# Optimization experiments

Hardware: AMD Instinct MI355X
Metric: run time of the kernel (lower is better)

## Reference

```python
import jax, jax.numpy as jnp
import numpy as np

EPS = 1e-5

def layer_norm(x, g, b):
    m = x.mean(-1, keepdims=True)
    v = ((x - m) ** 2).mean(-1, keepdims=True)
    return (x - m) * jax.lax.rsqrt(v + EPS) * g + b

def setup_inputs() -> dict:
    key = jax.random.key(0)
    ks = jax.random.split(key, 12)
    H = 2048; E = 2048; I = 2048; N = 32
    A = (H + E) // 2  # attention hidden = 2048
    s = lambda fan: 1.0 / np.sqrt(fan)
    inp = {
        "input":   jax.random.normal(ks[0], (I,), jnp.float32),
        "hiddens": jax.random.normal(ks[1], (N, H), jnp.float32),
        "cells":   jax.random.normal(ks[2], (N, H), jnp.float32),
        "external":jax.random.normal(ks[3], (E,), jnp.float32),
        # weights (torch nn.Linear layout: [out, in]); LN enabled -> no biases on linears
        "W_ai":   jax.random.uniform(ks[4], (A, H + E), jnp.float32, -s(H+E), s(H+E)),
        "W_attn": jax.random.uniform(ks[5], (1, A), jnp.float32, -s(A), s(A)),
        "W_merge":jax.random.uniform(ks[6], (H, H), jnp.float32, -s(H), s(H)),
        "W_iou":  jax.random.uniform(ks[7], (3 * H, I + H), jnp.float32, -s(I+H), s(I+H)),
        "W_fi":   jax.random.uniform(ks[8], (H, I), jnp.float32, -s(I), s(I)),
        "W_fh":   jax.random.uniform(ks[9], (H, H), jnp.float32, -s(H), s(H)),
        "g_merge": jnp.ones((H,), jnp.float32), "b_merge": jnp.zeros((H,), jnp.float32),
        "g_f": jnp.ones((H,), jnp.float32), "b_f": jnp.zeros((H,), jnp.float32),
        "g_i": jnp.ones((H,), jnp.float32), "b_i": jnp.zeros((H,), jnp.float32),
        "g_o": jnp.ones((H,), jnp.float32), "b_o": jnp.zeros((H,), jnp.float32),
        "g_u": jnp.ones((H,), jnp.float32), "b_u": jnp.zeros((H,), jnp.float32),
        "g_c": jnp.ones((H,), jnp.float32), "b_c": jnp.zeros((H,), jnp.float32),
    }
    return inp

def reference(input, hiddens, cells, external,
              W_ai, W_attn, W_merge, W_iou, W_fi, W_fh,
              g_merge, b_merge, g_f, b_f, g_i, b_i, g_o, b_o, g_u, b_u, g_c, b_c):
    N, H = hiddens.shape
    # forget-gate preactivations: [H] + [N,H] -> [N,H]
    f_lin = input @ W_fi.T + hiddens @ W_fh.T
    # attentive merge over children
    ext = jnp.broadcast_to(external, (N, external.shape[0]))
    ai = jnp.tanh(jnp.concatenate([hiddens, ext], axis=1) @ W_ai.T)       # [N, (H+E)//2]
    attn = jax.nn.softmax(ai @ W_attn.T, axis=0)                          # [N, 1]
    merged = (hiddens * attn).sum(0)                                      # [H]
    merge_hidden = jnp.tanh(layer_norm(merged @ W_merge.T, g_merge, b_merge))
    # i/o/u gates from [input ; merged_hidden]
    iou = jnp.concatenate([input, merge_hidden]) @ W_iou.T                # [3H]
    i_l, o_l, u_l = jnp.split(iou, 3)
    f = jax.nn.sigmoid(layer_norm(f_lin, g_f, b_f))                       # [N,H]
    i = jax.nn.sigmoid(layer_norm(i_l, g_i, b_i))
    o = jax.nn.sigmoid(layer_norm(o_l, g_o, b_o))
    u = jnp.tanh(layer_norm(u_l, g_u, b_u))                               # dropout=0 -> identity
    new_cell = layer_norm(i * u + (f * cells).sum(0), g_c, b_c)           # [H]
    new_h = o * jnp.tanh(new_cell)
    return new_h, new_cell
```

## Files before the change

### kernel.cpp

```cpp
#include <hip/hip_runtime.h>
#include <hip/hip_bf16.h>

typedef __bf16 bf16_t;
typedef __attribute__((ext_vector_type(8))) __bf16 bf16x8;
typedef __attribute__((ext_vector_type(4))) float f32x4;

#define EPSF 1e-5f

__global__ __launch_bounds__(256) void s1_mega(
    const float* __restrict__ hiddens, const float* __restrict__ external,
    const float* __restrict__ input,
    const float* __restrict__ W_ai, const float* __restrict__ W_fh,
    const float* __restrict__ W_fi, const float* __restrict__ W_attn,
    float* __restrict__ lp, float* __restrict__ fh_out, float* __restrict__ fi_out)
{
    __shared__ float red[4][16][16];
    __shared__ float ejs[4][16];

    int b    = blockIdx.x;
    int tid  = threadIdx.x;
    int wave = tid >> 6;
    int lane = tid & 63;

    if (b < 512) {
        bool is_ai = (b < 256);
        int  bb    = is_ai ? b : b - 256;
        int  jt    = bb & 127;
        int  nt    = bb >> 7;
        int  l15   = lane & 15;
        int  quad  = lane >> 4;
        int  k0    = wave * 512;
        int  wstride = is_ai ? 4096 : 2048;
        const float* W = is_ai ? W_ai : W_fh;

        const float* ap = hiddens + (size_t)(nt * 16 + l15) * 2048 + quad * 8 + k0;
        const float* bp = W + (size_t)(jt * 16 + l15) * wstride + quad * 8 + k0;

        f32x4 acc = {0.f, 0.f, 0.f, 0.f};
        float ejacc = 0.f;

        if (is_ai) {
            const float* ep = bp + 2048;
            const float* xp = external + quad * 8 + k0;
            for (int k = 0; k < 512; k += 32) {
                float4 a0 = *(const float4*)(ap + k);
                float4 a1 = *(const float4*)(ap + k + 4);
                float4 b0 = *(const float4*)(bp + k);
                float4 b1 = *(const float4*)(bp + k + 4);
                bf16x8 av, bv;
                av[0]=(bf16_t)a0.x; av[1]=(bf16_t)a0.y; av[2]=(bf16_t)a0.z; av[3]=(bf16_t)a0.w;
                av[4]=(bf16_t)a1.x; av[5]=(bf16_t)a1.y; av[6]=(bf16_t)a1.z; av[7]=(bf16_t)a1.w;
                bv[0]=(bf16_t)b0.x; bv[1]=(bf16_t)b0.y; bv[2]=(bf16_t)b0.z; bv[3]=(bf16_t)b0.w;
                bv[4]=(bf16_t)b1.x; bv[5]=(bf16_t)b1.y; bv[6]=(bf16_t)b1.z; bv[7]=(bf16_t)b1.w;
                acc = __builtin_amdgcn_mfma_f32_16x16x32_bf16(av, bv, acc, 0, 0, 0);
                float4 e0 = *(const float4*)(ep + k);
                float4 e1 = *(const float4*)(ep + k + 4);
                float4 x0 = *(const float4*)(xp + k);
                float4 x1 = *(const float4*)(xp + k + 4);
                ejacc += e0.x*x0.x + e0.y*x0.y + e0.z*x0.z + e0.w*x0.w
                       + e1.x*x1.x + e1.y*x1.y + e1.z*x1.z + e1.w*x1.w;
            }
            ejacc += __shfl_xor(ejacc, 16, 64);
            ejacc += __shfl_xor(ejacc, 32, 64);
            if (quad == 0) ejs[wave][l15] = ejacc;
        } else {
            for (int k = 0; k < 512; k += 32) {
                float4 a0 = *(const float4*)(ap + k);
                float4 a1 = *(const float4*)(ap + k + 4);
                float4 b0 = *(const float4*)(bp + k);
                float4 b1 = *(const float4*)(bp + k + 4);
                bf16x8 av, bv;
                av[0]=(bf16_t)a0.x; av[1]=(bf16_t)a0.y; av[2]=(bf16_t)a0.z; av[3]=(bf16_t)a0.w;
                av[4]=(bf16_t)a1.x; av[5]=(bf16_t)a1.y; av[6]=(bf16_t)a1.z; av[7]=(bf16_t)a1.w;
                bv[0]=(bf16_t)b0.x; bv[1]=(bf16_t)b0.y; bv[2]=(bf16_t)b0.z; bv[3]=(bf16_t)b0.w;
                bv[4]=(bf16_t)b1.x; bv[5]=(bf16_t)b1.y; bv[6]=(bf16_t)b1.z; bv[7]=(bf16_t)b1.w;
                acc = __builtin_amdgcn_mfma_f32_16x16x32_bf16(av, bv, acc, 0, 0, 0);
            }
        }

        #pragma unroll
        for (int r = 0; r < 4; ++r) red[wave][quad * 4 + r][l15] = acc[r];
        __syncthreads();

        int row = tid >> 4, col = tid & 15;
        float s = red[0][row][col] + red[1][row][col] + red[2][row][col] + red[3][row][col];

        if (is_ai) {
            float ej = ejs[0][col] + ejs[1][col] + ejs[2][col] + ejs[3][col];
            float lg = tanhf(s + ej) * W_attn[jt * 16 + col];
            lg += __shfl_xor(lg, 1, 64);
            lg += __shfl_xor(lg, 2, 64);
            lg += __shfl_xor(lg, 4, 64);
            lg += __shfl_xor(lg, 8, 64);
            if (col == 0) lp[jt * 32 + nt * 16 + row] = lg;
        } else {
            fh_out[(size_t)(nt * 16 + row) * 2048 + jt * 16 + col] = s;
        }
    } else {
        int b2 = b - 512;
        #pragma unroll
        for (int r = 0; r < 4; ++r) {
            int row = b2 * 16 + wave * 4 + r;
            const float4* wp = (const float4*)(W_fi + (size_t)row * 2048) + lane;
            const float4* xp = (const float4*)input + lane;
            float acc2 = 0.f;
            #pragma unroll
            for (int k = 0; k < 512; k += 64) {
                float4 w = wp[k];
                float4 v = xp[k];
                acc2 += w.x*v.x + w.y*v.y + w.z*v.z + w.w*v.w;
            }
            #pragma unroll
            for (int off = 32; off; off >>= 1) acc2 += __shfl_down(acc2, off, 64);
            if (lane == 0) fi_out[row] = acc2;
        }
    }
}

__global__ __launch_bounds__(256) void s2_mega(
    const float* __restrict__ fi, const float* __restrict__ fh,
    const float* __restrict__ lp, const float* __restrict__ hiddens,
    float* __restrict__ frs, float* __restrict__ merged)
{
    __shared__ float s1[256], s2[256];
    int b = blockIdx.x, t = threadIdx.x;

    if (b < 32) {
        int n = b;
        float sum = 0.f, sq = 0.f;
        #pragma unroll
        for (int i = 0; i < 8; ++i) {
            int h = t * 8 + i;
            float v = fi[h] + fh[n * 2048 + h];
            sum += v; sq += v * v;
        }
        s1[t] = sum; s2[t] = sq;
        __syncthreads();
        for (int off = 128; off; off >>= 1) {
            if (t < off) { s1[t] += s1[t + off]; s2[t] += s2[t + off]; }
            __syncthreads();
        }
        if (t == 0) {
            const float inv = 1.f / 2048.f;
            float mean = s1[0] * inv;
            frs[n * 2]     = mean;
            frs[n * 2 + 1] = rsqrtf(s2[0] * inv - mean * mean + EPSF);
        }
    } else {
        __shared__ float lred[32][8];
        __shared__ float attnw[32];
        int n = t >> 3, sl = t & 7;
        float p = 0.f;
        #pragma unroll
        for (int m = 0; m < 16; ++m) p += lp[(sl * 16 + m) * 32 + n];
        lred[n][sl] = p;
        __syncthreads();
        if (sl == 0) {
            float lg = 0.f;
            #pragma unroll
            for (int m = 0; m < 8; ++m) lg += lred[n][m];
            lred[n][0] = lg;
        }
        __syncthreads();
        if (t < 32) {
            float mx = -1e30f;
            for (int m = 0; m < 32; ++m) mx = fmaxf(mx, lred[m][0]);
            float ssum = 0.f;
            for (int m = 0; m < 32; ++m) ssum += expf(lred[m][0] - mx);
            attnw[t] = expf(lred[t][0] - mx) / ssum;
        }
        __syncthreads();
        int h = (b - 32) * 256 + t;
        float acc = 0.f;
        #pragma unroll 8
        for (int n2 = 0; n2 < 32; ++n2) acc += attnw[n2] * hiddens[n2 * 2048 + h];
        merged[h] = acc;
    }
}

__global__ __launch_bounds__(256) void s3_mega(
    const float* __restrict__ W_merge, const float* __restrict__ merged,
    const float* __restrict__ fi, const float* __restrict__ fh,
    const float* __restrict__ frs, const float* __restrict__ gf,
    const float* __restrict__ bf_, const float* __restrict__ cells,
    float* __restrict__ mm, float* __restrict__ fc)
{
    int b = blockIdx.x, t = threadIdx.x;
    if (b < 512) {
        int row  = b * 4 + (t >> 6);
        int lane = t & 63;
        const float4* wp = (const float4*)(W_merge + (size_t)row * 2048) + lane;
        const float4* xp = (const float4*)merged + lane;
        float acc = 0.f;
        #pragma unroll
        for (int k = 0; k < 512; k += 64) {
            float4 w = wp[k];
            float4 v = xp[k];
            acc += w.x*v.x + w.y*v.y + w.z*v.z + w.w*v.w;
        }
        #pragma unroll
        for (int off = 32; off; off >>= 1) acc += __shfl_down(acc, off, 64);
        if (lane == 0) mm[row] = acc;
    } else {
        int h = (b - 512) * 256 + t;
        float g = gf[h], bb = bf_[h], f_i = fi[h];
        float acc = 0.f;
        for (int n = 0; n < 32; ++n) {
            float v = (f_i + fh[n * 2048 + h] - frs[n * 2]) * frs[n * 2 + 1] * g + bb;
            float f = 1.f / (1.f + expf(-v));
            acc += f * cells[n * 2048 + h];
        }
        fc[h] = acc;
    }
}

__global__ __launch_bounds__(256) void s4_iou(
    const float* __restrict__ W_iou, const float* __restrict__ mm,
    const float* __restrict__ input, const float* __restrict__ g,
    const float* __restrict__ bvec, float* __restrict__ iou)
{
    __shared__ float xcat[4096];
    __shared__ float s1[256], s2[256];
    int b = blockIdx.x, t = threadIdx.x;

    float v[8]; float sum = 0.f, sq = 0.f;
    #pragma unroll
    for (int i = 0; i < 8; ++i) {
        v[i] = mm[t * 8 + i]; sum += v[i]; sq += v[i] * v[i];
    }
    s1[t] = sum; s2[t] = sq;
    __syncthreads();
    for (int off = 128; off; off >>= 1) {
        if (t < off) { s1[t] += s1[t + off]; s2[t] += s2[t + off]; }
        __syncthreads();
    }
    const float inv = 1.f / 2048.f;
    float mean = s1[0] * inv;
    float r = rsqrtf(s2[0] * inv - mean * mean + EPSF);
    #pragma unroll
    for (int i = 0; i < 8; ++i) {
        int h = t * 8 + i;
        xcat[h]        = input[h];
        xcat[2048 + h] = tanhf((v[i] - mean) * r * g[h] + bvec[h]);
    }
    __syncthreads();

    int wave = t >> 6, lane = t & 63;
    #pragma unroll
    for (int rr = 0; rr < 4; ++rr) {
        int row = b * 16 + wave * 4 + rr;
        const float4* wp = (const float4*)(W_iou + (size_t)row * 4096) + lane;
        const float4* xp = (const float4*)xcat + lane;
        float acc = 0.f;
        #pragma unroll
        for (int k = 0; k < 1024; k += 64) {
            float4 w = wp[k];
            float4 x = xp[k];
            acc += w.x*x.x + w.y*x.y + w.z*x.z + w.w*x.w;
        }
        #pragma unroll
        for (int off = 32; off; off >>= 1) acc += __shfl_down(acc, off, 64);
        if (lane == 0) iou[row] = acc;
    }
}

__global__ __launch_bounds__(256) void s5_tail(
    const float* __restrict__ iou, const float* __restrict__ fc,
    const float* __restrict__ gi, const float* __restrict__ bi,
    const float* __restrict__ go, const float* __restrict__ bo,
    const float* __restrict__ gu, const float* __restrict__ bu,
    const float* __restrict__ gc, const float* __restrict__ bc,
    float* __restrict__ out)
{
    __shared__ float sA[6][256];
    int t = threadIdx.x;
    float vi[8], vo[8], vu[8];
    float si = 0, qi = 0, so = 0, qo = 0, su = 0, qu = 0;
    #pragma unroll
    for (int i = 0; i < 8; ++i) {
        int h = t * 8 + i;
        vi[i] = iou[h]; vo[i] = iou[2048 + h]; vu[i] = iou[4096 + h];
        si += vi[i]; qi += vi[i] * vi[i];
        so += vo[i]; qo += vo[i] * vo[i];
        su += vu[i]; qu += vu[i] * vu[i];
    }
    sA[0][t] = si; sA[1][t] = qi; sA[2][t] = so;
    sA[3][t] = qo; sA[4][t] = su; sA[5][t] = qu;
    __syncthreads();
    for (int off = 128; off; off >>= 1) {
        if (t < off) {
            #pragma unroll
            for (int c = 0; c < 6; ++c) sA[c][t] += sA[c][t + off];
        }
        __syncthreads();
    }
    const float inv = 1.f / 2048.f;
    float mi = sA[0][0] * inv, ri = rsqrtf(sA[1][0] * inv - mi * mi + EPSF);
    float mo = sA[2][0] * inv, ro = rsqrtf(sA[3][0] * inv - mo * mo + EPSF);
    float mu = sA[4][0] * inv, ru = rsqrtf(sA[5][0] * inv - mu * mu + EPSF);
    __syncthreads();

    float o_[8], v_[8];
    float sv = 0, qv = 0;
    #pragma unroll
    for (int i = 0; i < 8; ++i) {
        int h = t * 8 + i;
        float ivl = 1.f / (1.f + expf(-((vi[i] - mi) * ri * gi[h] + bi[h])));
        o_[i]     = 1.f / (1.f + expf(-((vo[i] - mo) * ro * go[h] + bo[h])));
        float uvl = tanhf((vu[i] - mu) * ru * gu[h] + bu[h]);
        v_[i] = ivl * uvl + fc[h];
        sv += v_[i]; qv += v_[i] * v_[i];
    }
    sA[0][t] = sv; sA[1][t] = qv;
    __syncthreads();
    for (int off = 128; off; off >>= 1) {
        if (t < off) { sA[0][t] += sA[0][t + off]; sA[1][t] += sA[1][t + off]; }
        __syncthreads();
    }
    float mc = sA[0][0] * inv, rc = rsqrtf(sA[1][0] * inv - mc * mc + EPSF);
    #pragma unroll
    for (int i = 0; i < 8; ++i) {
        int h = t * 8 + i;
        float nc = (v_[i] - mc) * rc * gc[h] + bc[h];
        float nh = o_[i] * tanhf(nc);
        out[h]        = nh;
        out[2048 + h] = nc;
    }
}

extern "C" void kernel_launch(void* const* d_in, const int* in_sizes, int n_in,
                              void* d_out, int out_size, void* d_ws, size_t ws_size,
                              hipStream_t stream)
{
    const float* input    = (const float*)d_in[0];
    const float* hiddens  = (const float*)d_in[1];
    const float* cells    = (const float*)d_in[2];
    const float* external = (const float*)d_in[3];
    const float* W_ai     = (const float*)d_in[4];
    const float* W_attn   = (const float*)d_in[5];
    const float* W_merge  = (const float*)d_in[6];
    const float* W_iou    = (const float*)d_in[7];
    const float* W_fi     = (const float*)d_in[8];
    const float* W_fh     = (const float*)d_in[9];
    const float* g_merge  = (const float*)d_in[10];
    const float* b_merge  = (const float*)d_in[11];
    const float* g_f      = (const float*)d_in[12];
    const float* b_f      = (const float*)d_in[13];
    const float* g_i      = (const float*)d_in[14];
    const float* b_i      = (const float*)d_in[15];
    const float* g_o      = (const float*)d_in[16];
    const float* b_o      = (const float*)d_in[17];
    const float* g_u      = (const float*)d_in[18];
    const float* b_u      = (const float*)d_in[19];
    const float* g_c      = (const float*)d_in[20];
    const float* b_c      = (const float*)d_in[21];

    float* ws = (float*)d_ws;
    float* ws_fh     = ws;
    float* ws_fi     = ws + 65536;
    float* ws_lp     = ws + 67584;
    float* ws_frs    = ws + 71680;
    float* ws_merged = ws + 71744;
    float* ws_mm     = ws + 73792;
    float* ws_fc     = ws + 75840;
    float* ws_iou    = ws + 77888;
    float* out = (float*)d_out;

    s1_mega<<<640, 256, 0, stream>>>(hiddens, external, input,
                                     W_ai, W_fh, W_fi, W_attn,
                                     ws_lp, ws_fh, ws_fi);
    s2_mega<<<40, 256, 0, stream>>>(ws_fi, ws_fh, ws_lp, hiddens,
                                    ws_frs, ws_merged);
    s3_mega<<<520, 256, 0, stream>>>(W_merge, ws_merged, ws_fi, ws_fh,
                                     ws_frs, g_f, b_f, cells, ws_mm, ws_fc);
    s4_iou<<<384, 256, 0, stream>>>(W_iou, ws_mm, input, g_merge, b_merge, ws_iou);
    s5_tail<<<1, 256, 0, stream>>>(ws_iou, ws_fc, g_i, b_i, g_o, b_o,
                                   g_u, b_u, g_c, b_c, out);
}
```

Before: 279.7 us.

## Fuse five stage kernels into one cooperative kernel with grid syncs

Replaces the five separate stage launches with a single cooperative kernel of 512 blocks that separates the stages with grid.sync(). The goal is to remove per-launch overhead and the gaps between kernels in this latency-bound, memory-streaming workload. Each MFMA block now computes both 16-row halves of the batch, reusing each loaded weight tile twice, and the per-block row counts of the GEMV stages are rebalanced to fit the smaller grid. In exchange the grid is capped at the co-resident limit of 2 blocks per CU, some stages leave many blocks idle, and each grid barrier has its own cost.

Result: slower. 534.8 us (+91.2%).

```diff
diff --git a/kernel.cpp b/kernel.cpp
--- a/kernel.cpp
+++ b/kernel.cpp
@@ -1,5 +1,8 @@
 #include <hip/hip_runtime.h>
 #include <hip/hip_bf16.h>
+#include <hip/hip_cooperative_groups.h>
+
+namespace cg = cooperative_groups;
 
 typedef __bf16 bf16_t;
 typedef __attribute__((ext_vector_type(8))) __bf16 bf16x8;
@@ -7,52 +10,64 @@
 
 #define EPSF 1e-5f
 
-__global__ __launch_bounds__(256) void s1_mega(
-    const float* __restrict__ hiddens, const float* __restrict__ external,
-    const float* __restrict__ input,
-    const float* __restrict__ W_ai, const float* __restrict__ W_fh,
-    const float* __restrict__ W_fi, const float* __restrict__ W_attn,
-    float* __restrict__ lp, float* __restrict__ fh_out, float* __restrict__ fi_out)
+#define CVT8(dst, s0, s1)                                                      \
+    dst[0]=(bf16_t)s0.x; dst[1]=(bf16_t)s0.y; dst[2]=(bf16_t)s0.z; dst[3]=(bf16_t)s0.w; \
+    dst[4]=(bf16_t)s1.x; dst[5]=(bf16_t)s1.y; dst[6]=(bf16_t)s1.z; dst[7]=(bf16_t)s1.w;
+
+__global__ __launch_bounds__(256, 2) void mega(
+    const float* __restrict__ input, const float* __restrict__ hiddens,
+    const float* __restrict__ cells, const float* __restrict__ external,
+    const float* __restrict__ W_ai, const float* __restrict__ W_attn,
+    const float* __restrict__ W_merge, const float* __restrict__ W_iou,
+    const float* __restrict__ W_fi, const float* __restrict__ W_fh,
+    const float* __restrict__ g_merge, const float* __restrict__ b_merge,
+    const float* __restrict__ g_f, const float* __restrict__ b_f,
+    const float* __restrict__ g_i, const float* __restrict__ b_i,
+    const float* __restrict__ g_o, const float* __restrict__ b_o,
+    const float* __restrict__ g_u, const float* __restrict__ b_u,
+    const float* __restrict__ g_c, const float* __restrict__ b_c,
+    float* __restrict__ lp, float* __restrict__ fh_out, float* __restrict__ fi_out,
+    float* __restrict__ frs, float* __restrict__ merged, float* __restrict__ mm,
+    float* __restrict__ fc, float* __restrict__ iou, float* __restrict__ out)
 {
-    __shared__ float red[4][16][16];
-    __shared__ float ejs[4][16];
-
-    int b    = blockIdx.x;
-    int tid  = threadIdx.x;
-    int wave = tid >> 6;
-    int lane = tid & 63;
-
-    if (b < 512) {
-        bool is_ai = (b < 256);
-        int  bb    = is_ai ? b : b - 256;
-        int  jt    = bb & 127;
-        int  nt    = bb >> 7;
-        int  l15   = lane & 15;
-        int  quad  = lane >> 4;
-        int  k0    = wave * 512;
-        int  wstride = is_ai ? 4096 : 2048;
-        const float* W = is_ai ? W_ai : W_fh;
-
-        const float* ap = hiddens + (size_t)(nt * 16 + l15) * 2048 + quad * 8 + k0;
-        const float* bp = W + (size_t)(jt * 16 + l15) * wstride + quad * 8 + k0;
-
-        f32x4 acc = {0.f, 0.f, 0.f, 0.f};
-        float ejacc = 0.f;
+    cg::grid_group grid = cg::this_grid();
+    __shared__ __align__(16) float sm[4608];
+
+    const int b    = blockIdx.x;
+    const int tid  = threadIdx.x;
+    const int wave = tid >> 6;
+    const int lane = tid & 63;
+
+    if (b < 256) {
+        const bool is_ai = (b < 128);
+        const int  jt    = is_ai ? b : b - 128;
+        const int  l15   = lane & 15;
+        const int  quad  = lane >> 4;
+        const int  k0    = wave * 512;
+        const int  wstride = is_ai ? 4096 : 2048;
+        const float* W  = is_ai ? W_ai : W_fh;
+
+        const float* ap0 = hiddens + (size_t)l15 * 2048 + quad * 8 + k0;
+        const float* ap1 = ap0 + 16 * 2048;
+        const float* bp  = W + (size_t)(jt * 16 + l15) * wstride + quad * 8 + k0;
+
+        f32x4 acc0 = {0.f,0.f,0.f,0.f}, acc1 = {0.f,0.f,0.f,0.f};
 
         if (is_ai) {
             const float* ep = bp + 2048;
             const float* xp = external + quad * 8 + k0;
+            float ejacc = 0.f;
             for (int k = 0; k < 512; k += 32) {
-                float4 a0 = *(const float4*)(ap + k);
-                float4 a1 = *(const float4*)(ap + k + 4);
                 float4 b0 = *(const float4*)(bp + k);
                 float4 b1 = *(const float4*)(bp + k + 4);
-                bf16x8 av, bv;
-                av[0]=(bf16_t)a0.x; av[1]=(bf16_t)a0.y; av[2]=(bf16_t)a0.z; av[3]=(bf16_t)a0.w;
-                av[4]=(bf16_t)a1.x; av[5]=(bf16_t)a1.y; av[6]=(bf16_t)a1.z; av[7]=(bf16_t)a1.w;
-                bv[0]=(bf16_t)b0.x; bv[1]=(bf16_t)b0.y; bv[2]=(bf16_t)b0.z; bv[3]=(bf16_t)b0.w;
-                bv[4]=(bf16_t)b1.x; bv[5]=(bf16_t)b1.y; bv[6]=(bf16_t)b1.z; bv[7]=(bf16_t)b1.w;
-                acc = __builtin_amdgcn_mfma_f32_16x16x32_bf16(av, bv, acc, 0, 0, 0);
+                float4 a0 = *(const float4*)(ap0 + k);
+                float4 a1 = *(const float4*)(ap0 + k + 4);
+                float4 c0 = *(const float4*)(ap1 + k);
+                float4 c1 = *(const float4*)(ap1 + k + 4);
+                bf16x8 bv, av0, av1;
+                CVT8(bv, b0, b1); CVT8(av0, a0, a1); CVT8(av1, c0, c1);
+                acc0 = __builtin_amdgcn_mfma_f32_16x16x32_bf16(av0, bv, acc0, 0, 0, 0);
+                acc1 = __builtin_amdgcn_mfma_f32_16x16x32_bf16(av1, bv, acc1, 0, 0, 0);
                 float4 e0 = *(const float4*)(ep + k);
                 float4 e1 = *(const float4*)(ep + k + 4);
                 float4 x0 = *(const float4*)(xp + k);
@@ -62,269 +77,251 @@
             }
             ejacc += __shfl_xor(ejacc, 16, 64);
             ejacc += __shfl_xor(ejacc, 32, 64);
-            if (quad == 0) ejs[wave][l15] = ejacc;
+            if (quad == 0) sm[2048 + wave * 16 + l15] = ejacc;
         } else {
             for (int k = 0; k < 512; k += 32) {
-                float4 a0 = *(const float4*)(ap + k);
-                float4 a1 = *(const float4*)(ap + k + 4);
                 float4 b0 = *(const float4*)(bp + k);
                 float4 b1 = *(const float4*)(bp + k + 4);
-                bf16x8 av, bv;
-                av[0]=(bf16_t)a0.x; av[1]=(bf16_t)a0.y; av[2]=(bf16_t)a0.z; av[3]=(bf16_t)a0.w;
-                av[4]=(bf16_t)a1.x; av[5]=(bf16_t)a1.y; av[6]=(bf16_t)a1.z; av[7]=(bf16_t)a1.w;
-                bv[0]=(bf16_t)b0.x; bv[1]=(bf16_t)b0.y; bv[2]=(bf16_t)b0.z; bv[3]=(bf16_t)b0.w;
-                bv[4]=(bf16_t)b1.x; bv[5]=(bf16_t)b1.y; bv[6]=(bf16_t)b1.z; bv[7]=(bf16_t)b1.w;
-                acc = __builtin_amdgcn_mfma_f32_16x16x32_bf16(av, bv, acc, 0, 0, 0);
-            }
-        }
-
-        #pragma unroll
-        for (int r = 0; r < 4; ++r) red[wave][quad * 4 + r][l15] = acc[r];
+                float4 a0 = *(const float4*)(ap0 + k);
+                float4 a1 = *(const float4*)(ap0 + k + 4);
+                float4 c0 = *(const float4*)(ap1 + k);
+                float4 c1 = *(const float4*)(ap1 + k + 4);
+                bf16x8 bv, av0, av1;
+                CVT8(bv, b0, b1); CVT8(av0, a0, a1); CVT8(av1, c0, c1);
+                acc0 = __builtin_amdgcn_mfma_f32_16x16x32_bf16(av0, bv, acc0, 0, 0, 0);
+                acc1 = __builtin_amdgcn_mfma_f32_16x16x32_bf16(av1, bv, acc1, 0, 0, 0);
+            }
+        }
+
+        #pragma unroll
+        for (int r = 0; r < 4; ++r) {
+            sm[wave * 512 +       (quad * 4 + r) * 16 + l15] = acc0[r];
+            sm[wave * 512 + 256 + (quad * 4 + r) * 16 + l15] = acc1[r];
+        }
         __syncthreads();
 
         int row = tid >> 4, col = tid & 15;
-        float s = red[0][row][col] + red[1][row][col] + red[2][row][col] + red[3][row][col];
+        float s0  = sm[row*16+col]     + sm[512+row*16+col]
+                  + sm[1024+row*16+col] + sm[1536+row*16+col];
+        float s1v = sm[256+row*16+col] + sm[768+row*16+col]
+                  + sm[1280+row*16+col] + sm[1792+row*16+col];
 
         if (is_ai) {
-            float ej = ejs[0][col] + ejs[1][col] + ejs[2][col] + ejs[3][col];
-            float lg = tanhf(s + ej) * W_attn[jt * 16 + col];
-            lg += __shfl_xor(lg, 1, 64);
-            lg += __shfl_xor(lg, 2, 64);
-            lg += __shfl_xor(lg, 4, 64);
-            lg += __shfl_xor(lg, 8, 64);
-            if (col == 0) lp[jt * 32 + nt * 16 + row] = lg;
+            float ej = sm[2048+col] + sm[2064+col] + sm[2080+col] + sm[2096+col];
+            float wat = W_attn[jt * 16 + col];
+            float lg0 = tanhf(s0  + ej) * wat;
+            float lg1 = tanhf(s1v + ej) * wat;
+            #pragma unroll
+            for (int m = 1; m < 16; m <<= 1) {
+                lg0 += __shfl_xor(lg0, m, 64);
+                lg1 += __shfl_xor(lg1, m, 64);
+            }
+            if (col == 0) {
+                lp[jt * 32 + row]      = lg0;
+                lp[jt * 32 + 16 + row] = lg1;
+            }
         } else {
-            fh_out[(size_t)(nt * 16 + row) * 2048 + jt * 16 + col] = s;
+            fh_out[(size_t)row * 2048 + jt * 16 + col]        = s0;
+            fh_out[(size_t)(16 + row) * 2048 + jt * 16 + col] = s1v;
         }
     } else {
-        int b2 = b - 512;
-        #pragma unroll
-        for (int r = 0; r < 4; ++r) {
-            int row = b2 * 16 + wave * 4 + r;
+        int bb = b - 256;
+        #pragma unroll
+        for (int r = 0; r < 2; ++r) {
+            int row = bb * 8 + wave * 2 + r;
             const float4* wp = (const float4*)(W_fi + (size_t)row * 2048) + lane;
             const float4* xp = (const float4*)input + lane;
-            float acc2 = 0.f;
+            float a = 0.f;
             #pragma unroll
             for (int k = 0; k < 512; k += 64) {
-                float4 w = wp[k];
-                float4 v = xp[k];
-                acc2 += w.x*v.x + w.y*v.y + w.z*v.z + w.w*v.w;
-            }
-            #pragma unroll
-            for (int off = 32; off; off >>= 1) acc2 += __shfl_down(acc2, off, 64);
-            if (lane == 0) fi_out[row] = acc2;
-        }
-    }
-}
-
-__global__ __launch_bounds__(256) void s2_mega(
-    const float* __restrict__ fi, const float* __restrict__ fh,
-    const float* __restrict__ lp, const float* __restrict__ hiddens,
-    float* __restrict__ frs, float* __restrict__ merged)
-{
-    __shared__ float s1[256], s2[256];
-    int b = blockIdx.x, t = threadIdx.x;
+                float4 w = wp[k], v = xp[k];
+                a += w.x*v.x + w.y*v.y + w.z*v.z + w.w*v.w;
+            }
+            #pragma unroll
+            for (int off = 32; off; off >>= 1) a += __shfl_down(a, off, 64);
+            if (lane == 0) fi_out[row] = a;
+        }
+    }
+    grid.sync();
 
     if (b < 32) {
+        float* s1 = sm; float* s2 = sm + 256;
         int n = b;
         float sum = 0.f, sq = 0.f;
         #pragma unroll
         for (int i = 0; i < 8; ++i) {
-            int h = t * 8 + i;
-            float v = fi[h] + fh[n * 2048 + h];
+            int h = tid * 8 + i;
+            float v = fi_out[h] + fh_out[n * 2048 + h];
             sum += v; sq += v * v;
         }
-        s1[t] = sum; s2[t] = sq;
+        s1[tid] = sum; s2[tid] = sq;
         __syncthreads();
         for (int off = 128; off; off >>= 1) {
-            if (t < off) { s1[t] += s1[t + off]; s2[t] += s2[t + off]; }
+            if (tid < off) { s1[tid] += s1[tid + off]; s2[tid] += s2[tid + off]; }
             __syncthreads();
         }
-        if (t == 0) {
+        if (tid == 0) {
             const float inv = 1.f / 2048.f;
             float mean = s1[0] * inv;
             frs[n * 2]     = mean;
             frs[n * 2 + 1] = rsqrtf(s2[0] * inv - mean * mean + EPSF);
         }
-    } else {
-        __shared__ float lred[32][8];
-        __shared__ float attnw[32];
-        int n = t >> 3, sl = t & 7;
+    } else if (b < 40) {
+        float* lred  = sm;
+        float* attnw = sm + 256;
+        int n = tid >> 3, sl = tid & 7;
         float p = 0.f;
         #pragma unroll
         for (int m = 0; m < 16; ++m) p += lp[(sl * 16 + m) * 32 + n];
-        lred[n][sl] = p;
+        lred[n * 8 + sl] = p;
         __syncthreads();
         if (sl == 0) {
             float lg = 0.f;
             #pragma unroll
-            for (int m = 0; m < 8; ++m) lg += lred[n][m];
-            lred[n][0] = lg;
-        }
-        __syncthreads();
-        if (t < 32) {
+            for (int m = 0; m < 8; ++m) lg += lred[n * 8 + m];
+            lred[n * 8] = lg;
+        }
+        __syncthreads();
+        if (tid < 32) {
             float mx = -1e30f;
-            for (int m = 0; m < 32; ++m) mx = fmaxf(mx, lred[m][0]);
+            for (int m = 0; m < 32; ++m) mx = fmaxf(mx, lred[m * 8]);
             float ssum = 0.f;
-            for (int m = 0; m < 32; ++m) ssum += expf(lred[m][0] - mx);
-            attnw[t] = expf(lred[t][0] - mx) / ssum;
-        }
-        __syncthreads();
-        int h = (b - 32) * 256 + t;
+            for (int m = 0; m < 32; ++m) ssum += expf(lred[m * 8] - mx);
+            attnw[tid] = expf(lred[tid * 8] - mx) / ssum;
+        }
+        __syncthreads();
+        int h = (b - 32) * 256 + tid;
         float acc = 0.f;
         #pragma unroll 8
         for (int n2 = 0; n2 < 32; ++n2) acc += attnw[n2] * hiddens[n2 * 2048 + h];
         merged[h] = acc;
     }
-}
-
-__global__ __launch_bounds__(256) void s3_mega(
-    const float* __restrict__ W_merge, const float* __restrict__ merged,
-    const float* __restrict__ fi, const float* __restrict__ fh,
-    const float* __restrict__ frs, const float* __restrict__ gf,
-    const float* __restrict__ bf_, const float* __restrict__ cells,
-    float* __restrict__ mm, float* __restrict__ fc)
-{
-    int b = blockIdx.x, t = threadIdx.x;
-    if (b < 512) {
-        int row  = b * 4 + (t >> 6);
-        int lane = t & 63;
-        const float4* wp = (const float4*)(W_merge + (size_t)row * 2048) + lane;
-        const float4* xp = (const float4*)merged + lane;
-        float acc = 0.f;
-        #pragma unroll
-        for (int k = 0; k < 512; k += 64) {
-            float4 w = wp[k];
-            float4 v = xp[k];
-            acc += w.x*v.x + w.y*v.y + w.z*v.z + w.w*v.w;
-        }
-        #pragma unroll
-        for (int off = 32; off; off >>= 1) acc += __shfl_down(acc, off, 64);
-        if (lane == 0) mm[row] = acc;
-    } else {
-        int h = (b - 512) * 256 + t;
-        float g = gf[h], bb = bf_[h], f_i = fi[h];
+    grid.sync();
+
+    if (b < 256) {
+        #pragma unroll
+        for (int r = 0; r < 2; ++r) {
+            int row = b * 8 + wave * 2 + r;
+            const float4* wp = (const float4*)(W_merge + (size_t)row * 2048) + lane;
+            const float4* xp = (const float4*)merged + lane;
+            float a = 0.f;
+            #pragma unroll
+            for (int k = 0; k < 512; k += 64) {
+                float4 w = wp[k], v = xp[k];
+                a += w.x*v.x + w.y*v.y + w.z*v.z + w.w*v.w;
+            }
+            #pragma unroll
+            for (int off = 32; off; off >>= 1) a += __shfl_down(a, off, 64);
+            if (lane == 0) mm[row] = a;
+        }
+    } else if (b < 264) {
+        int h = (b - 256) * 256 + tid;
+        float g = g_f[h], bb2 = b_f[h], f_i = fi_out[h];
         float acc = 0.f;
         for (int n = 0; n < 32; ++n) {
-            float v = (f_i + fh[n * 2048 + h] - frs[n * 2]) * frs[n * 2 + 1] * g + bb;
-            float f = 1.f / (1.f + expf(-v));
-            acc += f * cells[n * 2048 + h];
+            float v = (f_i + fh_out[n * 2048 + h] - frs[n * 2]) * frs[n * 2 + 1] * g + bb2;
+            acc += (1.f / (1.f + expf(-v))) * cells[n * 2048 + h];
         }
         fc[h] = acc;
     }
-}
-
-__global__ __launch_bounds__(256) void s4_iou(
-    const float* __restrict__ W_iou, const float* __restrict__ mm,
-    const float* __restrict__ input, const float* __restrict__ g,
-    const float* __restrict__ bvec, float* __restrict__ iou)
-{
-    __shared__ float xcat[4096];
-    __shared__ float s1[256], s2[256];
-    int b = blockIdx.x, t = threadIdx.x;
-
-    float v[8]; float sum = 0.f, sq = 0.f;
-    #pragma unroll
-    for (int i = 0; i < 8; ++i) {
-        v[i] = mm[t * 8 + i]; sum += v[i]; sq += v[i] * v[i];
-    }
-    s1[t] = sum; s2[t] = sq;
-    __syncthreads();
-    for (int off = 128; off; off >>= 1) {
-        if (t < off) { s1[t] += s1[t + off]; s2[t] += s2[t + off]; }
-        __syncthreads();
-    }
-    const float inv = 1.f / 2048.f;
-    float mean = s1[0] * inv;
-    float r = rsqrtf(s2[0] * inv - mean * mean + EPSF);
-    #pragma unroll
-    for (int i = 0; i < 8; ++i) {
-        int h = t * 8 + i;
-        xcat[h]        = input[h];
-        xcat[2048 + h] = tanhf((v[i] - mean) * r * g[h] + bvec[h]);
-    }
-    __syncthreads();
-
-    int wave = t >> 6, lane = t & 63;
-    #pragma unroll
-    for (int rr = 0; rr < 4; ++rr) {
-        int row = b * 16 + wave * 4 + rr;
-        const float4* wp = (const float4*)(W_iou + (size_t)row * 4096) + lane;
-        const float4* xp = (const float4*)xcat + lane;
-        float acc = 0.f;
-        #pragma unroll
-        for (int k = 0; k < 1024; k += 64) {
-            float4 w = wp[k];
-            float4 x = xp[k];
-            acc += w.x*x.x + w.y*x.y + w.z*x.z + w.w*x.w;
-        }
-        #pragma unroll
-        for (int off = 32; off; off >>= 1) acc += __shfl_down(acc, off, 64);
-        if (lane == 0) iou[row] = acc;
-    }
-}
-
-__global__ __launch_bounds__(256) void s5_tail(
-    const float* __restrict__ iou, const float* __restrict__ fc,
-    const float* __restrict__ gi, const float* __restrict__ bi,
-    const float* __restrict__ go, const float* __restrict__ bo,
-    const float* __restrict__ gu, const float* __restrict__ bu,
-    const float* __restrict__ gc, const float* __restrict__ bc,
-    float* __restrict__ out)
-{
-    __shared__ float sA[6][256];
-    int t = threadIdx.x;
-    float vi[8], vo[8], vu[8];
-    float si = 0, qi = 0, so = 0, qo = 0, su = 0, qu = 0;
-    #pragma unroll
-    for (int i = 0; i < 8; ++i) {
-        int h = t * 8 + i;
-        vi[i] = iou[h]; vo[i] = iou[2048 + h]; vu[i] = iou[4096 + h];
-        si += vi[i]; qi += vi[i] * vi[i];
-        so += vo[i]; qo += vo[i] * vo[i];
-        su += vu[i]; qu += vu[i] * vu[i];
-    }
-    sA[0][t] = si; sA[1][t] = qi; sA[2][t] = so;
-    sA[3][t] = qo; sA[4][t] = su; sA[5][t] = qu;
-    __syncthreads();
-    for (int off = 128; off; off >>= 1) {
-        if (t < off) {
-            #pragma unroll
-            for (int c = 0; c < 6; ++c) sA[c][t] += sA[c][t + off];
-        }
-        __syncthreads();
-    }
-    const float inv = 1.f / 2048.f;
-    float mi = sA[0][0] * inv, ri = rsqrtf(sA[1][0] * inv - mi * mi + EPSF);
-    float mo = sA[2][0] * inv, ro = rsqrtf(sA[3][0] * inv - mo * mo + EPSF);
-    float mu = sA[4][0] * inv, ru = rsqrtf(sA[5][0] * inv - mu * mu + EPSF);
-    __syncthreads();
-
-    float o_[8], v_[8];
-    float sv = 0, qv = 0;
-    #pragma unroll
-    for (int i = 0; i < 8; ++i) {
-        int h = t * 8 + i;
-        float ivl = 1.f / (1.f + expf(-((vi[i] - mi) * ri * gi[h] + bi[h])));
-        o_[i]     = 1.f / (1.f + expf(-((vo[i] - mo) * ro * go[h] + bo[h])));
-        float uvl = tanhf((vu[i] - mu) * ru * gu[h] + bu[h]);
-        v_[i] = ivl * uvl + fc[h];
-        sv += v_[i]; qv += v_[i] * v_[i];
-    }
-    sA[0][t] = sv; sA[1][t] = qv;
-    __syncthreads();
-    for (int off = 128; off; off >>= 1) {
-        if (t < off) { sA[0][t] += sA[0][t + off]; sA[1][t] += sA[1][t + off]; }
-        __syncthreads();
-    }
-    float mc = sA[0][0] * inv, rc = rsqrtf(sA[1][0] * inv - mc * mc + EPSF);
-    #pragma unroll
-    for (int i = 0; i < 8; ++i) {
-        int h = t * 8 + i;
-        float nc = (v_[i] - mc) * rc * gc[h] + bc[h];
-        float nh = o_[i] * tanhf(nc);
-        out[h]        = nh;
-        out[2048 + h] = nc;
+    grid.sync();
+
+    {
+        float* xcat = sm;
+        float* s1 = sm + 4096; float* s2 = sm + 4352;
+        float v[8]; float sum = 0.f, sq = 0.f;
+        #pragma unroll
+        for (int i = 0; i < 8; ++i) {
+            v[i] = mm[tid * 8 + i]; sum += v[i]; sq += v[i] * v[i];
+        }
+        s1[tid] = sum; s2[tid] = sq;
+        __syncthreads();
+        for (int off = 128; off; off >>= 1) {
+            if (tid < off) { s1[tid] += s1[tid + off]; s2[tid] += s2[tid + off]; }
+            __syncthreads();
+        }
+        const float inv = 1.f / 2048.f;
+        float mean = s1[0] * inv;
+        float r = rsqrtf(s2[0] * inv - mean * mean + EPSF);
+        #pragma unroll
+        for (int i = 0; i < 8; ++i) {
+            int h = tid * 8 + i;
+            xcat[h]        = input[h];
+            xcat[2048 + h] = tanhf((v[i] - mean) * r * g_merge[h] + b_merge[h]);
+        }
+        __syncthreads();
+
+        #pragma unroll
+        for (int rr = 0; rr < 3; ++rr) {
+            int row = b * 12 + wave * 3 + rr;
+            const float4* wp = (const float4*)(W_iou + (size_t)row * 4096) + lane;
+            const float4* xp = (const float4*)xcat + lane;
+            float a = 0.f;
+            #pragma unroll
+            for (int k = 0; k < 1024; k += 64) {
+                float4 w = wp[k], x = xp[k];
+                a += w.x*x.x + w.y*x.y + w.z*x.z + w.w*x.w;
+            }
+            #pragma unroll
+            for (int off = 32; off; off >>= 1) a += __shfl_down(a, off, 64);
+            if (lane == 0) iou[row] = a;
+        }
+    }
+    grid.sync();
+
+    if (b == 0) {
+        int t = tid;
+        float vi[8], vo[8], vu[8];
+        float si = 0, qi = 0, so = 0, qo = 0, su = 0, qu = 0;
+        #pragma unroll
+        for (int i = 0; i < 8; ++i) {
+            int h = t * 8 + i;
+            vi[i] = iou[h]; vo[i] = iou[2048 + h]; vu[i] = iou[4096 + h];
+            si += vi[i]; qi += vi[i] * vi[i];
+            so += vo[i]; qo += vo[i] * vo[i];
+            su += vu[i]; qu += vu[i] * vu[i];
+        }
+        sm[t] = si; sm[256 + t] = qi; sm[512 + t] = so;
+        sm[768 + t] = qo; sm[1024 + t] = su; sm[1280 + t] = qu;
+        __syncthreads();
+        for (int off = 128; off; off >>= 1) {
+            if (t < off) {
+                #pragma unroll
+                for (int c = 0; c < 6; ++c) sm[c * 256 + t] += sm[c * 256 + t + off];
+            }
+            __syncthreads();
+        }
+        const float inv = 1.f / 2048.f;
+        float mi = sm[0] * inv,    ri = rsqrtf(sm[256] * inv - mi * mi + EPSF);
+        float mo = sm[512] * inv,  ro = rsqrtf(sm[768] * inv - mo * mo + EPSF);
+        float mu = sm[1024] * inv, ru = rsqrtf(sm[1280] * inv - mu * mu + EPSF);
+        __syncthreads();
+
+        float o_[8], v_[8];
+        float sv = 0, qv = 0;
+        #pragma unroll
+        for (int i = 0; i < 8; ++i) {
+            int h = t * 8 + i;
+            float ivl = 1.f / (1.f + expf(-((vi[i] - mi) * ri * g_i[h] + b_i[h])));
+            o_[i]     = 1.f / (1.f + expf(-((vo[i] - mo) * ro * g_o[h] + b_o[h])));
+            float uvl = tanhf((vu[i] - mu) * ru * g_u[h] + b_u[h]);
+            v_[i] = ivl * uvl + fc[h];
+            sv += v_[i]; qv += v_[i] * v_[i];
+        }
+        sm[t] = sv; sm[256 + t] = qv;
+        __syncthreads();
+        for (int off = 128; off; off >>= 1) {
+            if (t < off) { sm[t] += sm[t + off]; sm[256 + t] += sm[256 + t + off]; }
+            __syncthreads();
+        }
+        float mc = sm[0] * inv, rc = rsqrtf(sm[256] * inv - mc * mc + EPSF);
+        #pragma unroll
+        for (int i = 0; i < 8; ++i) {
+            int h = t * 8 + i;
+            float nc = (v_[i] - mc) * rc * g_c[h] + b_c[h];
+            out[h]        = o_[i] * tanhf(nc);
+            out[2048 + h] = nc;
+        }
     }
 }
 
@@ -356,9 +353,9 @@
     const float* b_c      = (const float*)d_in[21];
 
     float* ws = (float*)d_ws;
-    float* ws_fh     = ws;
-    float* ws_fi     = ws + 65536;
-    float* ws_lp     = ws + 67584;
+    float* ws_lp     = ws;
+    float* ws_fh     = ws + 4096;
+    float* ws_fi     = ws + 69632;
     float* ws_frs    = ws + 71680;
     float* ws_merged = ws + 71744;
     float* ws_mm     = ws + 73792;
@@ -366,14 +363,16 @@
     float* ws_iou    = ws + 77888;
     float* out = (float*)d_out;
 
-    s1_mega<<<640, 256, 0, stream>>>(hiddens, external, input,
-                                     W_ai, W_fh, W_fi, W_attn,
-                                     ws_lp, ws_fh, ws_fi);
-    s2_mega<<<40, 256, 0, stream>>>(ws_fi, ws_fh, ws_lp, hiddens,
-                                    ws_frs, ws_merged);
-    s3_mega<<<520, 256, 0, stream>>>(W_merge, ws_merged, ws_fi, ws_fh,
-                                     ws_frs, g_f, b_f, cells, ws_mm, ws_fc);
-    s4_iou<<<384, 256, 0, stream>>>(W_iou, ws_mm, input, g_merge, b_merge, ws_iou);
-    s5_tail<<<1, 256, 0, stream>>>(ws_iou, ws_fc, g_i, b_i, g_o, b_o,
-                                   g_u, b_u, g_c, b_c, out);
+    void* args[] = {
+        (void*)&input, (void*)&hiddens, (void*)&cells, (void*)&external,
+        (void*)&W_ai, (void*)&W_attn, (void*)&W_merge, (void*)&W_iou,
+        (void*)&W_fi, (void*)&W_fh,
+        (void*)&g_merge, (void*)&b_merge, (void*)&g_f, (void*)&b_f,
+        (void*)&g_i, (void*)&b_i, (void*)&g_o, (void*)&b_o,
+        (void*)&g_u, (void*)&b_u, (void*)&g_c, (void*)&b_c,
+        (void*)&ws_lp, (void*)&ws_fh, (void*)&ws_fi, (void*)&ws_frs,
+        (void*)&ws_merged, (void*)&ws_mm, (void*)&ws_fc, (void*)&ws_iou,
+        (void*)&out
+    };
+    hipLaunchCooperativeKernel((void*)mega, dim3(512), dim3(256), args, 0, stream);
 }
```
